# Kernel optimization log

Hardware: AMD Instinct MI355X
Metric: run time of the kernel (lower is better)

The kernel has to match this reference:

```python
import jax, jax.numpy as jnp
import numpy as np

N = 50000      # nodes
E = 250000     # edges
NG = 2500      # graphs
H = 32         # atom_dim
ND = 32        # node feature dim
ED = 16        # edge feature dim
CONV_N = 3     # message passing steps
EMB_STEPS = 3  # Set2Set processing steps


def setup_inputs() -> dict:
    key = jax.random.key(0)
    ks = jax.random.split(key, 16)
    w = lambda k, shape, s=0.05: jax.random.normal(k, shape, jnp.float32) * s
    return {
        "x": jax.random.normal(ks[0], (N, ND), jnp.float32),
        "edge_index": jax.random.randint(ks[1], (2, E), 0, N),
        "edge_attr": jax.random.normal(ks[2], (E, ED), jnp.float32),
        "batch": jnp.sort(jax.random.randint(ks[3], (N,), 0, NG)),
        "lin_w": w(ks[4], (ND, H)), "lin_b": jnp.zeros((H,), jnp.float32),
        "e_w1": w(ks[5], (ED, 2 * H)), "e_b1": jnp.zeros((2 * H,), jnp.float32),
        "e_w2": w(ks[6], (2 * H, H * H)), "e_b2": jnp.zeros((H * H,), jnp.float32),
        "gru_w_ih": w(ks[7], (3 * H, H)), "gru_w_hh": w(ks[8], (3 * H, H)),
        "gru_b_ih": jnp.zeros((3 * H,), jnp.float32), "gru_b_hh": jnp.zeros((3 * H,), jnp.float32),
        "lstm_w_ih": w(ks[9], (4 * H, 2 * H)), "lstm_w_hh": w(ks[10], (4 * H, H)),
        "lstm_b_ih": jnp.zeros((4 * H,), jnp.float32), "lstm_b_hh": jnp.zeros((4 * H,), jnp.float32),
        "pred_w": w(ks[11], (2 * H, 1)), "pred_b": jnp.zeros((1,), jnp.float32),
    }


def _mpnn_forward(x, edge_attr, lin_w, lin_b, e_w1, e_b1, e_w2, e_b2,
                  gru_w_ih, gru_w_hh, gru_b_ih, gru_b_hh,
                  lstm_w_ih, lstm_w_hh, lstm_b_ih, lstm_b_hh,
                  pred_w, pred_b, edge_index, batch):
    src, dst = edge_index[0], edge_index[1]
    # initial node embedding: relu(Linear(node_dim -> atom_dim))
    out = jax.nn.relu(x @ lin_w + lin_b)            # [N, H]
    h = out                                         # GRU hidden state [N, H]

    # edge-conditioned weights (edge MLP output is constant across conv steps)
    e_h = jax.nn.relu(edge_attr @ e_w1 + e_b1)      # [E, 2H]
    W_e = (e_h @ e_w2 + e_b2).reshape(E, H, H)      # [E, H, H]

    # mean-aggregation denominator per target node
    deg = jax.ops.segment_sum(jnp.ones((E,), out.dtype), dst, num_segments=N)
    denom = jnp.maximum(deg, 1.0)[:, None]          # [N, 1]

    for _ in range(CONV_N):
        # NNConv message: m_e = x_src @ W_e, mean-scattered to dst
        msg = jnp.einsum('eh,eho->eo', out[src], W_e)                   # [E, H]
        agg = jax.ops.segment_sum(msg, dst, num_segments=N) / denom     # [N, H]
        m = jax.nn.relu(agg)
        # single GRU cell step (seq_len=1)
        gi = m @ gru_w_ih.T + gru_b_ih              # [N, 3H]
        gh = h @ gru_w_hh.T + gru_b_hh              # [N, 3H]
        i_r, i_z, i_n = jnp.split(gi, 3, axis=-1)
        h_r, h_z, h_n = jnp.split(gh, 3, axis=-1)
        r = jax.nn.sigmoid(i_r + h_r)
        z = jax.nn.sigmoid(i_z + h_z)
        n = jnp.tanh(i_n + r * h_n)
        h = (1.0 - z) * n + z * h
        out = h

    # Set2Set pooling over graphs (only last embedding used, residual='last')
    q_star = jnp.zeros((NG, 2 * H), out.dtype)
    hl = jnp.zeros((NG, H), out.dtype)
    cl = jnp.zeros((NG, H), out.dtype)
    for _ in range(EMB_STEPS):
        g = q_star @ lstm_w_ih.T + lstm_b_ih + hl @ lstm_w_hh.T + lstm_b_hh  # [NG, 4H]
        gi_, gf_, gg_, go_ = jnp.split(g, 4, axis=-1)
        i_g = jax.nn.sigmoid(gi_)
        f_g = jax.nn.sigmoid(gf_)
        g_g = jnp.tanh(gg_)
        o_g = jax.nn.sigmoid(go_)
        cl = f_g * cl + i_g * g_g
        hl = o_g * jnp.tanh(cl)
        q = hl                                       # [NG, H]
        e = jnp.sum(out * q[batch], axis=-1)         # [N]
        e_max = jax.ops.segment_max(e, batch, num_segments=NG)
        e_exp = jnp.exp(e - e_max[batch])
        e_den = jax.ops.segment_sum(e_exp, batch, num_segments=NG)
        a = e_exp / e_den[batch]                     # softmax within each graph
        r_pool = jax.ops.segment_sum(a[:, None] * out, batch, num_segments=NG)  # [NG, H]
        q_star = jnp.concatenate([q, r_pool], axis=-1)

    pred = q_star @ pred_w + pred_b                  # [NG, 1]
    return pred.reshape(-1)


def reference(x, edge_index, edge_attr, batch, lin_w, lin_b, e_w1, e_b1, e_w2, e_b2,
              gru_w_ih, gru_w_hh, gru_b_ih, gru_b_hh,
              lstm_w_ih, lstm_w_hh, lstm_b_ih, lstm_b_hh, pred_w, pred_b):
    return _mpnn_forward(x, edge_attr, lin_w, lin_b, e_w1, e_b1, e_w2, e_b2,
                         gru_w_ih, gru_w_hh, gru_b_ih, gru_b_hh,
                         lstm_w_ih, lstm_w_hh, lstm_b_ih, lstm_b_hh,
                         pred_w, pred_b, edge_index, batch)
```

## Files before the change

### kernel.cpp

```cpp
#include <hip/hip_runtime.h>
#include <hip/hip_bf16.h>

namespace {
constexpr int kN = 50000;
constexpr int kE = 250000;
constexpr int kG = 2500;
constexpr int NB = 8;

__device__ __forceinline__ float sigmoidf_(float x) { return 1.0f / (1.0f + expf(-x)); }

__global__ void k_starts(const int* __restrict__ batch, int* __restrict__ starts) {
  int g = blockIdx.x * blockDim.x + threadIdx.x;
  if (g > kG) return;
  int lo = 0, hi = kN;
  while (lo < hi) {
    int mid = (lo + hi) >> 1;
    if (batch[mid] < g) lo = mid + 1; else hi = mid;
  }
  starts[g] = lo;
}

__global__ __launch_bounds__(256) void k_node_init(const float* __restrict__ x,
                                                   const float* __restrict__ lin_w,
                                                   const float* __restrict__ lin_b,
                                                   float* __restrict__ h) {
  __shared__ float ws[32 * 32];
  __shared__ float bs[32];
  for (int i = threadIdx.x; i < 1024; i += 256) ws[i] = lin_w[i];
  if (threadIdx.x < 32) bs[threadIdx.x] = lin_b[threadIdx.x];
  __syncthreads();
  int n = blockIdx.x * 256 + threadIdx.x;
  if (n >= kN) return;
  float xv[32];
  const float4* xp = (const float4*)(x + (size_t)n * 32);
#pragma unroll
  for (int i = 0; i < 8; ++i) {
    float4 v = xp[i];
    xv[4 * i + 0] = v.x; xv[4 * i + 1] = v.y; xv[4 * i + 2] = v.z; xv[4 * i + 3] = v.w;
  }
  float acc[32];
#pragma unroll
  for (int o = 0; o < 32; ++o) acc[o] = bs[o];
  for (int i = 0; i < 32; ++i) {
    float a = xv[i];
    const float4* wr = (const float4*)&ws[i * 32];
#pragma unroll
    for (int o4 = 0; o4 < 8; ++o4) {
      float4 w = wr[o4];
      acc[4 * o4 + 0] = fmaf(a, w.x, acc[4 * o4 + 0]);
      acc[4 * o4 + 1] = fmaf(a, w.y, acc[4 * o4 + 1]);
      acc[4 * o4 + 2] = fmaf(a, w.z, acc[4 * o4 + 2]);
      acc[4 * o4 + 3] = fmaf(a, w.w, acc[4 * o4 + 3]);
    }
  }
  float4* hp = (float4*)(h + (size_t)n * 32);
#pragma unroll
  for (int i = 0; i < 8; ++i) {
    float4 v;
    v.x = fmaxf(acc[4 * i + 0], 0.f);
    v.y = fmaxf(acc[4 * i + 1], 0.f);
    v.z = fmaxf(acc[4 * i + 2], 0.f);
    v.w = fmaxf(acc[4 * i + 3], 0.f);
    hp[i] = v;
  }
}

__global__ __launch_bounds__(256) void k_edge_h(const float* __restrict__ ea,
                                                const float* __restrict__ w1,
                                                const float* __restrict__ b1,
                                                const int* __restrict__ pos_of_e,
                                                float* __restrict__ ehs) {
  __shared__ float ws[16 * 64];
  __shared__ float bs[64];
  for (int i = threadIdx.x; i < 1024; i += 256) ws[i] = w1[i];
  if (threadIdx.x < 64) bs[threadIdx.x] = b1[threadIdx.x];
  __syncthreads();
  int e = blockIdx.x * 256 + threadIdx.x;
  if (e >= kE) return;
  float av[16];
  const float4* ap = (const float4*)(ea + (size_t)e * 16);
#pragma unroll
  for (int i = 0; i < 4; ++i) {
    float4 v = ap[i];
    av[4 * i + 0] = v.x; av[4 * i + 1] = v.y; av[4 * i + 2] = v.z; av[4 * i + 3] = v.w;
  }
  float acc[64];
#pragma unroll
  for (int o = 0; o < 64; ++o) acc[o] = bs[o];
  for (int i = 0; i < 16; ++i) {
    float a = av[i];
    const float4* wr = (const float4*)&ws[i * 64];
#pragma unroll
    for (int o4 = 0; o4 < 16; ++o4) {
      float4 w = wr[o4];
      acc[4 * o4 + 0] = fmaf(a, w.x, acc[4 * o4 + 0]);
      acc[4 * o4 + 1] = fmaf(a, w.y, acc[4 * o4 + 1]);
      acc[4 * o4 + 2] = fmaf(a, w.z, acc[4 * o4 + 2]);
      acc[4 * o4 + 3] = fmaf(a, w.w, acc[4 * o4 + 3]);
    }
  }
  float4* op = (float4*)(ehs + (size_t)pos_of_e[e] * 64);
#pragma unroll
  for (int i = 0; i < 16; ++i) {
    float4 v;
    v.x = fmaxf(acc[4 * i + 0], 0.f);
    v.y = fmaxf(acc[4 * i + 1], 0.f);
    v.z = fmaxf(acc[4 * i + 2], 0.f);
    v.w = fmaxf(acc[4 * i + 3], 0.f);
    op[i] = v;
  }
}

__global__ void k_hist2(const int* __restrict__ src, const int* __restrict__ dst,
                        int* __restrict__ cnt_s, int* __restrict__ cnt_d) {
  int e = blockIdx.x * blockDim.x + threadIdx.x;
  if (e < kE) {
    atomicAdd(&cnt_s[src[e]], 1);
    atomicAdd(&cnt_d[dst[e]], 1);
  }
}

__global__ __launch_bounds__(1024) void k_scan2(const int* __restrict__ cnt_s, int* __restrict__ offs_s,
                                                const int* __restrict__ cnt_d, int* __restrict__ offs_d) {
  const int* cnt = blockIdx.x ? cnt_d : cnt_s;
  int* offs = blockIdx.x ? offs_d : offs_s;
  __shared__ int wsum[16];
  __shared__ int wpre[16];
  __shared__ int carry_s;
  const int tid = threadIdx.x;
  const int lane = tid & 63, wv = tid >> 6;
  if (tid == 0) carry_s = 0;
  __syncthreads();
  for (int base = 0; base < kN; base += 1024) {
    int i = base + tid;
    int v = (i < kN) ? cnt[i] : 0;
    int x = v;
#pragma unroll
    for (int d = 1; d < 64; d <<= 1) {
      int t = __shfl_up(x, d, 64);
      if (lane >= d) x += t;
    }
    if (lane == 63) wsum[wv] = x;
    __syncthreads();
    if (wv == 0) {
      int y = (lane < 16) ? wsum[lane] : 0;
#pragma unroll
      for (int d = 1; d < 16; d <<= 1) {
        int t = __shfl_up(y, d, 64);
        if (lane >= d && lane < 16) y += t;
      }
      if (lane < 16) wpre[lane] = y - wsum[lane];
    }
    __syncthreads();
    int carry = carry_s;
    if (i < kN) offs[i] = carry + wpre[wv] + (x - v);
    __syncthreads();
    if (tid == 0) carry_s = carry + wpre[15] + wsum[15];
    __syncthreads();
  }
  if (tid == 0) offs[kN] = carry_s;
}

__global__ void k_scatter_s(const int* __restrict__ src, const int* __restrict__ dst,
                            const int* __restrict__ offs, int* __restrict__ cur,
                            unsigned char* __restrict__ es_nl, int* __restrict__ es_dst,
                            int* __restrict__ pos_of_e) {
  int e = blockIdx.x * blockDim.x + threadIdx.x;
  if (e >= kE) return;
  int s = src[e];
  int pos = offs[s] + atomicAdd(&cur[s], 1);
  es_nl[pos] = (unsigned char)(s & (NB - 1));
  es_dst[pos] = dst[e];
  pos_of_e[e] = pos;
}

__global__ void k_scatter_d(const int* __restrict__ es_dst, const int* __restrict__ offs_d,
                            int* __restrict__ cur_d, int* __restrict__ ed_pos) {
  int ei = blockIdx.x * blockDim.x + threadIdx.x;
  if (ei >= kE) return;
  int d = es_dst[ei];
  int pd = offs_d[d] + atomicAdd(&cur_d[d], 1);
  ed_pos[pd] = ei;
}

__global__ void k_w2t(const float* __restrict__ w2, float* __restrict__ w2t) {
  int i = blockIdx.x * 256 + threadIdx.x;
  if (i >= 65536) return;
  int k = i & 63, oa = i >> 6;
  int o = oa & 31, a = oa >> 5;
  w2t[i] = w2[(size_t)k * 1024 + a * 32 + o];
}

__global__ __launch_bounds__(256, 4) void k_conv3(const float* __restrict__ h,
                                                  const float* __restrict__ ehs,
                                                  const float* __restrict__ w2t,
                                                  const float* __restrict__ b2,
                                                  const unsigned char* __restrict__ es_nl,
                                                  const int* __restrict__ offs,
                                                  float* __restrict__ msgbuf) {
  __shared__ float Ts[NB][32][36];
  __shared__ float hs[NB][32];
  __shared__ float hb2[NB][32];
  const int n0 = blockIdx.x * NB;
  const int t = threadIdx.x;
  const int nloc = t >> 5, o32 = t & 31;
  hs[nloc][o32] = h[(size_t)(n0 + nloc) * 32 + o32];
  __syncthreads();
  {
    float a0 = 0.f;
#pragma unroll 8
    for (int a = 0; a < 32; ++a) a0 = fmaf(hs[nloc][a], b2[a * 32 + o32], a0);
    hb2[nloc][o32] = a0;
  }
  const int og = t >> 3;
  const int kq = t & 7;
  const int es = offs[n0], ee = offs[n0 + NB];
  const float* wp = w2t + og * 64 + kq * 4;

  for (int kh = 0; kh < 2; ++kh) {
    float4 acc[NB];
#pragma unroll
    for (int n = 0; n < NB; ++n) acc[n] = make_float4(0.f, 0.f, 0.f, 0.f);
    const float* wph = wp + kh * 32;
#pragma unroll 2
    for (int a4 = 0; a4 < 8; ++a4) {
      const float* wa = wph + (size_t)(a4 * 4) * 2048;
      float4 w0 = *(const float4*)(wa);
      float4 w1 = *(const float4*)(wa + 2048);
      float4 w2v = *(const float4*)(wa + 4096);
      float4 w3 = *(const float4*)(wa + 6144);
#pragma unroll
      for (int n = 0; n < NB; ++n) {
        float4 hv = *(const float4*)&hs[n][a4 * 4];
        acc[n].x = fmaf(hv.x, w0.x, acc[n].x); acc[n].y = fmaf(hv.x, w0.y, acc[n].y);
        acc[n].z = fmaf(hv.x, w0.z, acc[n].z); acc[n].w = fmaf(hv.x, w0.w, acc[n].w);
        acc[n].x = fmaf(hv.y, w1.x, acc[n].x); acc[n].y = fmaf(hv.y, w1.y, acc[n].y);
        acc[n].z = fmaf(hv.y, w1.z, acc[n].z); acc[n].w = fmaf(hv.y, w1.w, acc[n].w);
        acc[n].x = fmaf(hv.z, w2v.x, acc[n].x); acc[n].y = fmaf(hv.z, w2v.y, acc[n].y);
        acc[n].z = fmaf(hv.z, w2v.z, acc[n].z); acc[n].w = fmaf(hv.z, w2v.w, acc[n].w);
        acc[n].x = fmaf(hv.w, w3.x, acc[n].x); acc[n].y = fmaf(hv.w, w3.y, acc[n].y);
        acc[n].z = fmaf(hv.w, w3.z, acc[n].z); acc[n].w = fmaf(hv.w, w3.w, acc[n].w);
      }
    }
    if (kh) __syncthreads();
#pragma unroll
    for (int n = 0; n < NB; ++n) *(float4*)&Ts[n][og][kq * 4] = acc[n];
    __syncthreads();
    const int kg = t >> 5;
#pragma unroll 2
    for (int ei = es + kg; ei < ee; ei += 8) {
      const int nl = es_nl[ei];
      const float ehv = ehs[(size_t)ei * 64 + kh * 32 + o32];
      float m = kh ? msgbuf[(size_t)ei * 32 + o32] : hb2[nl][o32];
      const float* tp = &Ts[nl][o32][0];
#pragma unroll
      for (int j4 = 0; j4 < 8; ++j4) {
        float4 tv = *(const float4*)(tp + j4 * 4);
        m = fmaf(__shfl(ehv, j4 * 4 + 0, 32), tv.x, m);
        m = fmaf(__shfl(ehv, j4 * 4 + 1, 32), tv.y, m);
        m = fmaf(__shfl(ehv, j4 * 4 + 2, 32), tv.z, m);
        m = fmaf(__shfl(ehv, j4 * 4 + 3, 32), tv.w, m);
      }
      msgbuf[(size_t)ei * 32 + o32] = m;
    }
  }
}

__global__ __launch_bounds__(256) void k_agg(const float* __restrict__ msgbuf,
                                             const int* __restrict__ ed_pos,
                                             const int* __restrict__ offs_d,
                                             float* __restrict__ m_out) {
  int d = blockIdx.x * 8 + (threadIdx.x >> 5);
  if (d >= kN) return;
  int o = threadIdx.x & 31;
  int s = offs_d[d], e = offs_d[d + 1];
  float acc = 0.f;
  int j = s;
  for (; j + 1 < e; j += 2) {
    int p0 = ed_pos[j], p1 = ed_pos[j + 1];
    acc += msgbuf[(size_t)p0 * 32 + o] + msgbuf[(size_t)p1 * 32 + o];
  }
  if (j < e) acc += msgbuf[(size_t)ed_pos[j] * 32 + o];
  float dn = (float)(e - s);
  if (dn < 1.f) dn = 1.f;
  m_out[(size_t)d * 32 + o] = fmaxf(acc / dn, 0.f);
}

__global__ __launch_bounds__(256) void k_gru(float* __restrict__ h, const float* __restrict__ m_in,
                                             const float* __restrict__ Wih, const float* __restrict__ Whh,
                                             const float* __restrict__ bih, const float* __restrict__ bhh) {
  __shared__ float wih_s[96 * 32];
  __shared__ float whh_s[96 * 32];
  __shared__ float bih_s[96], bhh_s[96];
  for (int i = threadIdx.x; i < 96 * 32; i += 256) { wih_s[i] = Wih[i]; whh_s[i] = Whh[i]; }
  for (int i = threadIdx.x; i < 96; i += 256) { bih_s[i] = bih[i]; bhh_s[i] = bhh[i]; }
  __syncthreads();
  int n = blockIdx.x * 256 + threadIdx.x;
  if (n >= kN) return;
  float m[32], hv[32];
  const float4* ap = (const float4*)(m_in + (size_t)n * 32);
  const float4* hp = (const float4*)(h + (size_t)n * 32);
#pragma unroll
  for (int i = 0; i < 8; ++i) {
    float4 a = ap[i];
    m[4 * i + 0] = a.x; m[4 * i + 1] = a.y; m[4 * i + 2] = a.z; m[4 * i + 3] = a.w;
    float4 b = hp[i];
    hv[4 * i + 0] = b.x; hv[4 * i + 1] = b.y; hv[4 * i + 2] = b.z; hv[4 * i + 3] = b.w;
  }
  float rr[32], zz[32];
#pragma unroll 4
  for (int j = 0; j < 32; ++j) {
    float accA = bih_s[j], accB = bhh_s[j];
    const float4* wi = (const float4*)&wih_s[j * 32];
    const float4* wh = (const float4*)&whh_s[j * 32];
#pragma unroll
    for (int i = 0; i < 8; ++i) {
      float4 a = wi[i], b = wh[i];
      accA = fmaf(m[4 * i + 0], a.x, accA); accA = fmaf(m[4 * i + 1], a.y, accA);
      accA = fmaf(m[4 * i + 2], a.z, accA); accA = fmaf(m[4 * i + 3], a.w, accA);
      accB = fmaf(hv[4 * i + 0], b.x, accB); accB = fmaf(hv[4 * i + 1], b.y, accB);
      accB = fmaf(hv[4 * i + 2], b.z, accB); accB = fmaf(hv[4 * i + 3], b.w, accB);
    }
    rr[j] = sigmoidf_(accA + accB);
  }
#pragma unroll 4
  for (int j = 0; j < 32; ++j) {
    int row = 32 + j;
    float accA = bih_s[row], accB = bhh_s[row];
    const float4* wi = (const float4*)&wih_s[row * 32];
    const float4* wh = (const float4*)&whh_s[row * 32];
#pragma unroll
    for (int i = 0; i < 8; ++i) {
      float4 a = wi[i], b = wh[i];
      accA = fmaf(m[4 * i + 0], a.x, accA); accA = fmaf(m[4 * i + 1], a.y, accA);
      accA = fmaf(m[4 * i + 2], a.z, accA); accA = fmaf(m[4 * i + 3], a.w, accA);
      accB = fmaf(hv[4 * i + 0], b.x, accB); accB = fmaf(hv[4 * i + 1], b.y, accB);
      accB = fmaf(hv[4 * i + 2], b.z, accB); accB = fmaf(hv[4 * i + 3], b.w, accB);
    }
    zz[j] = sigmoidf_(accA + accB);
  }
#pragma unroll 4
  for (int j = 0; j < 32; ++j) {
    int row = 64 + j;
    float accA = bih_s[row], accB = bhh_s[row];
    const float4* wi = (const float4*)&wih_s[row * 32];
    const float4* wh = (const float4*)&whh_s[row * 32];
#pragma unroll
    for (int i = 0; i < 8; ++i) {
      float4 a = wi[i], b = wh[i];
      accA = fmaf(m[4 * i + 0], a.x, accA); accA = fmaf(m[4 * i + 1], a.y, accA);
      accA = fmaf(m[4 * i + 2], a.z, accA); accA = fmaf(m[4 * i + 3], a.w, accA);
      accB = fmaf(hv[4 * i + 0], b.x, accB); accB = fmaf(hv[4 * i + 1], b.y, accB);
      accB = fmaf(hv[4 * i + 2], b.z, accB); accB = fmaf(hv[4 * i + 3], b.w, accB);
    }
    float ng = tanhf(accA + rr[j] * accB);
    zz[j] = (1.f - zz[j]) * ng + zz[j] * hv[j];
  }
  float4* hw = (float4*)(h + (size_t)n * 32);
#pragma unroll
  for (int i = 0; i < 8; ++i)
    hw[i] = make_float4(zz[4 * i + 0], zz[4 * i + 1], zz[4 * i + 2], zz[4 * i + 3]);
}

__global__ __launch_bounds__(256) void k_s2s(const float* __restrict__ h,
                                             const int* __restrict__ starts,
                                             const float* __restrict__ lwih,
                                             const float* __restrict__ lwhh,
                                             const float* __restrict__ lbih,
                                             const float* __restrict__ lbhh,
                                             const float* __restrict__ pw,
                                             const float* __restrict__ pb,
                                             float* __restrict__ out) {
  __shared__ float wih_s[128][65];
  __shared__ float whh_s[128][33];
  __shared__ float bsum[128];
  for (int i = threadIdx.x; i < 128 * 64; i += 256) wih_s[i >> 6][i & 63] = lwih[i];
  for (int i = threadIdx.x; i < 128 * 32; i += 256) whh_s[i >> 5][i & 31] = lwhh[i];
  for (int i = threadIdx.x; i < 128; i += 256) bsum[i] = lbih[i] + lbhh[i];
  __syncthreads();
  const int g = blockIdx.x * 4 + (threadIdx.x >> 6);
  if (g >= kG) return;
  const int lane = threadIdx.x & 63;
  const int o = lane & 31;
  const int r1 = lane, r2 = lane + 64;
  const int s = starts[g], e = starts[g + 1];
  float c = 0.f, hl = 0.f, rp = 0.f;
  for (int step = 0; step < 3; ++step) {
    float v1 = bsum[r1], v2 = bsum[r2];
    for (int i = 0; i < 32; ++i) {
      float hli = __shfl(hl, i, 64);
      float rpi = __shfl(rp, i, 64);
      v1 = fmaf(wih_s[r1][i], hli, v1);
      v1 = fmaf(wih_s[r1][32 + i], rpi, v1);
      v1 = fmaf(whh_s[r1][i], hli, v1);
      v2 = fmaf(wih_s[r2][i], hli, v2);
      v2 = fmaf(wih_s[r2][32 + i], rpi, v2);
      v2 = fmaf(whh_s[r2][i], hli, v2);
    }
    float fg = sigmoidf_(__shfl(v1, 32 + o, 64));
    float og_ = sigmoidf_(__shfl(v2, 32 + o, 64));
    float ig = sigmoidf_(v1);
    float gg = tanhf(v2);
    c = fg * c + ig * gg;
    hl = og_ * tanhf(c);
    float q = __shfl(hl, o, 64);
    float mx = -3.0e38f;
    for (int nn = s; nn < e; nn += 2) {
      int n = nn + (lane >> 5);
      float val = (n < e) ? h[(size_t)n * 32 + o] * q : 0.f;
#pragma unroll
      for (int d = 16; d; d >>= 1) val += __shfl_xor(val, d, 32);
      if (n < e) mx = fmaxf(mx, val);
    }
    mx = fmaxf(mx, __shfl_xor(mx, 32, 64));
    float den = 0.f, racc = 0.f;
    for (int nn = s; nn < e; nn += 2) {
      int n = nn + (lane >> 5);
      float hvo = 0.f, val = 0.f;
      if (n < e) { hvo = h[(size_t)n * 32 + o]; val = hvo * q; }
#pragma unroll
      for (int d = 16; d; d >>= 1) val += __shfl_xor(val, d, 32);
      if (n < e) { float p = expf(val - mx); den += p; racc = fmaf(p, hvo, racc); }
    }
    den += __shfl_xor(den, 32, 64);
    racc += __shfl_xor(racc, 32, 64);
    rp = (e > s) ? racc / den : 0.f;
  }
  float acc = __shfl(hl, o, 64) * pw[o] + rp * pw[32 + o];
#pragma unroll
  for (int d = 16; d; d >>= 1) acc += __shfl_xor(acc, d, 32);
  if (lane == 0) out[g] = acc + pb[0];
}

}

extern "C" void kernel_launch(void* const* d_in, const int* in_sizes, int n_in,
                              void* d_out, int out_size, void* d_ws, size_t ws_size,
                              hipStream_t stream) {
  const float* x     = (const float*)d_in[0];
  const int*   eidx  = (const int*)d_in[1];
  const float* eattr = (const float*)d_in[2];
  const int*   batch = (const int*)d_in[3];
  const float* lin_w = (const float*)d_in[4];
  const float* lin_b = (const float*)d_in[5];
  const float* e_w1  = (const float*)d_in[6];
  const float* e_b1  = (const float*)d_in[7];
  const float* e_w2  = (const float*)d_in[8];
  const float* e_b2  = (const float*)d_in[9];
  const float* gwih  = (const float*)d_in[10];
  const float* gwhh  = (const float*)d_in[11];
  const float* gbih  = (const float*)d_in[12];
  const float* gbhh  = (const float*)d_in[13];
  const float* lwih  = (const float*)d_in[14];
  const float* lwhh  = (const float*)d_in[15];
  const float* lbih  = (const float*)d_in[16];
  const float* lbhh  = (const float*)d_in[17];
  const float* pw    = (const float*)d_in[18];
  const float* pb    = (const float*)d_in[19];
  const int* srcp = eidx;
  const int* dstp = eidx + kE;

  float* ws = (float*)d_ws;
  size_t off = 0;
  auto alloc = [&](size_t nel) {
    float* p = ws + off;
    off += (nel + 255) & ~(size_t)255;
    return p;
  };
  float* hbuf   = alloc((size_t)kN * 32);
  float* mbuf   = alloc((size_t)kN * 32);
  float* ehs    = alloc((size_t)kE * 64);
  float* msgbuf = alloc((size_t)kE * 32);
  float* w2t    = alloc(65536);
  int* starts   = (int*)alloc(kG + 1);
  int* cnt_s    = (int*)alloc(kN);
  int* cnt_d    = (int*)alloc(kN);
  int* cur_s    = (int*)alloc(kN);
  int* cur_d    = (int*)alloc(kN);
  int* offs_s   = (int*)alloc(kN + 1);
  int* offs_d   = (int*)alloc(kN + 1);
  int* es_dst   = (int*)alloc(kE);
  int* pos_of_e = (int*)alloc(kE);
  int* ed_pos   = (int*)alloc(kE);
  unsigned char* es_nl = (unsigned char*)alloc((kE + 3) / 4);
  if (ws_size / 4 < off) return;

  hipMemsetAsync(cnt_s, 0, (size_t)kN * 4, stream);
  hipMemsetAsync(cnt_d, 0, (size_t)kN * 4, stream);
  hipMemsetAsync(cur_s, 0, (size_t)kN * 4, stream);
  hipMemsetAsync(cur_d, 0, (size_t)kN * 4, stream);

  k_starts<<<(kG + 1 + 255) / 256, 256, 0, stream>>>(batch, starts);
  k_node_init<<<(kN + 255) / 256, 256, 0, stream>>>(x, lin_w, lin_b, hbuf);
  k_hist2<<<(kE + 255) / 256, 256, 0, stream>>>(srcp, dstp, cnt_s, cnt_d);
  k_scan2<<<2, 1024, 0, stream>>>(cnt_s, offs_s, cnt_d, offs_d);
  k_scatter_s<<<(kE + 255) / 256, 256, 0, stream>>>(srcp, dstp, offs_s, cur_s, es_nl, es_dst,
                                                    pos_of_e);
  k_edge_h<<<(kE + 255) / 256, 256, 0, stream>>>(eattr, e_w1, e_b1, pos_of_e, ehs);
  k_scatter_d<<<(kE + 255) / 256, 256, 0, stream>>>(es_dst, offs_d, cur_d, ed_pos);
  k_w2t<<<65536 / 256, 256, 0, stream>>>(e_w2, w2t);

  for (int step = 0; step < 3; ++step) {
    k_conv3<<<kN / NB, 256, 0, stream>>>(hbuf, ehs, w2t, e_b2, es_nl, offs_s, msgbuf);
    k_agg<<<(kN + 7) / 8, 256, 0, stream>>>(msgbuf, ed_pos, offs_d, mbuf);
    k_gru<<<(kN + 255) / 256, 256, 0, stream>>>(hbuf, mbuf, gwih, gwhh, gbih, gbhh);
  }

  k_s2s<<<(kG + 3) / 4, 256, 0, stream>>>(hbuf, starts, lwih, lwhh, lbih, lbhh, pw, pb,
                                          (float*)d_out);
}
```

Baseline: 1.004 ms.

## Restructure conv kernel with per-node edge loops, register-held transforms, coalesced edge_h writes

The conv kernel now assigns each warp one source node. Each lane keeps its row of the per-node transformed weight tile in registers and loops over that node's edges, reading edge hidden vectors as float4 instead of broadcasting them through shuffles. The shared tile uses an XOR swizzle, and weight loads are software-prefetched one step ahead. Edge-hidden computation now iterates in sorted edge order so its writes are coalesced, the aggregation loads destination indices cooperatively and shuffles them, and the GRU reads weights straight from global or cache instead of staging them in shared memory. The risk is load imbalance across warps when nodes have uneven degrees, and more register pressure.

```diff
diff --git a/kernel.cpp b/kernel.cpp
--- a/kernel.cpp
+++ b/kernel.cpp
@@ -68,15 +68,16 @@
 __global__ __launch_bounds__(256) void k_edge_h(const float* __restrict__ ea,
                                                 const float* __restrict__ w1,
                                                 const float* __restrict__ b1,
-                                                const int* __restrict__ pos_of_e,
+                                                const int* __restrict__ es_e,
                                                 float* __restrict__ ehs) {
   __shared__ float ws[16 * 64];
   __shared__ float bs[64];
   for (int i = threadIdx.x; i < 1024; i += 256) ws[i] = w1[i];
   if (threadIdx.x < 64) bs[threadIdx.x] = b1[threadIdx.x];
   __syncthreads();
-  int e = blockIdx.x * 256 + threadIdx.x;
-  if (e >= kE) return;
+  int pos = blockIdx.x * 256 + threadIdx.x;
+  if (pos >= kE) return;
+  int e = es_e[pos];
   float av[16];
   const float4* ap = (const float4*)(ea + (size_t)e * 16);
 #pragma unroll
@@ -99,7 +100,7 @@
       acc[4 * o4 + 3] = fmaf(a, w.w, acc[4 * o4 + 3]);
     }
   }
-  float4* op = (float4*)(ehs + (size_t)pos_of_e[e] * 64);
+  float4* op = (float4*)(ehs + (size_t)pos * 64);
 #pragma unroll
   for (int i = 0; i < 16; ++i) {
     float4 v;
@@ -163,15 +164,13 @@
 
 __global__ void k_scatter_s(const int* __restrict__ src, const int* __restrict__ dst,
                             const int* __restrict__ offs, int* __restrict__ cur,
-                            unsigned char* __restrict__ es_nl, int* __restrict__ es_dst,
-                            int* __restrict__ pos_of_e) {
+                            int* __restrict__ es_e, int* __restrict__ es_dst) {
   int e = blockIdx.x * blockDim.x + threadIdx.x;
   if (e >= kE) return;
   int s = src[e];
   int pos = offs[s] + atomicAdd(&cur[s], 1);
-  es_nl[pos] = (unsigned char)(s & (NB - 1));
+  es_e[pos] = e;
   es_dst[pos] = dst[e];
-  pos_of_e[e] = pos;
 }
 
 __global__ void k_scatter_d(const int* __restrict__ es_dst, const int* __restrict__ offs_d,
@@ -191,77 +190,87 @@
   w2t[i] = w2[(size_t)k * 1024 + a * 32 + o];
 }
 
-__global__ __launch_bounds__(256, 4) void k_conv3(const float* __restrict__ h,
+__global__ __launch_bounds__(256, 4) void k_conv4(const float* __restrict__ h,
                                                   const float* __restrict__ ehs,
                                                   const float* __restrict__ w2t,
                                                   const float* __restrict__ b2,
-                                                  const unsigned char* __restrict__ es_nl,
                                                   const int* __restrict__ offs,
                                                   float* __restrict__ msgbuf) {
   __shared__ float Ts[NB][32][36];
-  __shared__ float hs[NB][32];
-  __shared__ float hb2[NB][32];
   const int n0 = blockIdx.x * NB;
   const int t = threadIdx.x;
-  const int nloc = t >> 5, o32 = t & 31;
-  hs[nloc][o32] = h[(size_t)(n0 + nloc) * 32 + o32];
-  __syncthreads();
+  const int tb_o = t & 31;
+  const int tb_k = t >> 5;
+  const int eg_n = t >> 5;
+  const int eg_o = t & 31;
+  const int gs = offs[n0 + eg_n], ge = offs[n0 + eg_n + 1];
+
+  float hb2r = 0.f;
   {
-    float a0 = 0.f;
+    const float* hp = h + (size_t)(n0 + eg_n) * 32;
 #pragma unroll 8
-    for (int a = 0; a < 32; ++a) a0 = fmaf(hs[nloc][a], b2[a * 32 + o32], a0);
-    hb2[nloc][o32] = a0;
-  }
-  const int og = t >> 3;
-  const int kq = t & 7;
-  const int es = offs[n0], ee = offs[n0 + NB];
-  const float* wp = w2t + og * 64 + kq * 4;
+    for (int a = 0; a < 32; ++a) hb2r = fmaf(hp[a], b2[a * 32 + eg_o], hb2r);
+  }
+
+  const float* wp = w2t + tb_o * 64 + tb_k * 4;
+  const int tswz = tb_o >> 3;
+  const int rswz = eg_o >> 3;
 
   for (int kh = 0; kh < 2; ++kh) {
     float4 acc[NB];
 #pragma unroll
     for (int n = 0; n < NB; ++n) acc[n] = make_float4(0.f, 0.f, 0.f, 0.f);
     const float* wph = wp + kh * 32;
-#pragma unroll 2
+    float4 wa0 = *(const float4*)(wph);
+    float4 wa1 = *(const float4*)(wph + 2048);
+    float4 wa2 = *(const float4*)(wph + 4096);
+    float4 wa3 = *(const float4*)(wph + 6144);
+#pragma unroll
     for (int a4 = 0; a4 < 8; ++a4) {
-      const float* wa = wph + (size_t)(a4 * 4) * 2048;
-      float4 w0 = *(const float4*)(wa);
-      float4 w1 = *(const float4*)(wa + 2048);
-      float4 w2v = *(const float4*)(wa + 4096);
-      float4 w3 = *(const float4*)(wa + 6144);
+      const float* nx = wph + (size_t)((a4 < 7 ? a4 + 1 : a4) * 4) * 2048;
+      float4 wb0 = *(const float4*)(nx);
+      float4 wb1 = *(const float4*)(nx + 2048);
+      float4 wb2 = *(const float4*)(nx + 4096);
+      float4 wb3 = *(const float4*)(nx + 6144);
 #pragma unroll
       for (int n = 0; n < NB; ++n) {
-        float4 hv = *(const float4*)&hs[n][a4 * 4];
-        acc[n].x = fmaf(hv.x, w0.x, acc[n].x); acc[n].y = fmaf(hv.x, w0.y, acc[n].y);
-        acc[n].z = fmaf(hv.x, w0.z, acc[n].z); acc[n].w = fmaf(hv.x, w0.w, acc[n].w);
-        acc[n].x = fmaf(hv.y, w1.x, acc[n].x); acc[n].y = fmaf(hv.y, w1.y, acc[n].y);
-        acc[n].z = fmaf(hv.y, w1.z, acc[n].z); acc[n].w = fmaf(hv.y, w1.w, acc[n].w);
-        acc[n].x = fmaf(hv.z, w2v.x, acc[n].x); acc[n].y = fmaf(hv.z, w2v.y, acc[n].y);
-        acc[n].z = fmaf(hv.z, w2v.z, acc[n].z); acc[n].w = fmaf(hv.z, w2v.w, acc[n].w);
-        acc[n].x = fmaf(hv.w, w3.x, acc[n].x); acc[n].y = fmaf(hv.w, w3.y, acc[n].y);
-        acc[n].z = fmaf(hv.w, w3.z, acc[n].z); acc[n].w = fmaf(hv.w, w3.w, acc[n].w);
+        float4 hv = *(const float4*)(h + (size_t)(n0 + n) * 32 + a4 * 4);
+        acc[n].x = fmaf(hv.x, wa0.x, acc[n].x); acc[n].y = fmaf(hv.x, wa0.y, acc[n].y);
+        acc[n].z = fmaf(hv.x, wa0.z, acc[n].z); acc[n].w = fmaf(hv.x, wa0.w, acc[n].w);
+        acc[n].x = fmaf(hv.y, wa1.x, acc[n].x); acc[n].y = fmaf(hv.y, wa1.y, acc[n].y);
+        acc[n].z = fmaf(hv.y, wa1.z, acc[n].z); acc[n].w = fmaf(hv.y, wa1.w, acc[n].w);
+        acc[n].x = fmaf(hv.z, wa2.x, acc[n].x); acc[n].y = fmaf(hv.z, wa2.y, acc[n].y);
+        acc[n].z = fmaf(hv.z, wa2.z, acc[n].z); acc[n].w = fmaf(hv.z, wa2.w, acc[n].w);
+        acc[n].x = fmaf(hv.w, wa3.x, acc[n].x); acc[n].y = fmaf(hv.w, wa3.y, acc[n].y);
+        acc[n].z = fmaf(hv.w, wa3.z, acc[n].z); acc[n].w = fmaf(hv.w, wa3.w, acc[n].w);
       }
+      wa0 = wb0; wa1 = wb1; wa2 = wb2; wa3 = wb3;
     }
     if (kh) __syncthreads();
 #pragma unroll
-    for (int n = 0; n < NB; ++n) *(float4*)&Ts[n][og][kq * 4] = acc[n];
+    for (int n = 0; n < NB; ++n)
+      *(float4*)&Ts[n][tb_o][(tb_k ^ tswz) * 4] = acc[n];
     __syncthreads();
-    const int kg = t >> 5;
-#pragma unroll 2
-    for (int ei = es + kg; ei < ee; ei += 8) {
-      const int nl = es_nl[ei];
-      const float ehv = ehs[(size_t)ei * 64 + kh * 32 + o32];
-      float m = kh ? msgbuf[(size_t)ei * 32 + o32] : hb2[nl][o32];
-      const float* tp = &Ts[nl][o32][0];
-#pragma unroll
-      for (int j4 = 0; j4 < 8; ++j4) {
-        float4 tv = *(const float4*)(tp + j4 * 4);
-        m = fmaf(__shfl(ehv, j4 * 4 + 0, 32), tv.x, m);
-        m = fmaf(__shfl(ehv, j4 * 4 + 1, 32), tv.y, m);
-        m = fmaf(__shfl(ehv, j4 * 4 + 2, 32), tv.z, m);
-        m = fmaf(__shfl(ehv, j4 * 4 + 3, 32), tv.w, m);
+
+    if (gs < ge) {
+      float4 kv[8];
+#pragma unroll
+      for (int kq = 0; kq < 8; ++kq)
+        kv[kq] = *(const float4*)&Ts[eg_n][eg_o][(kq ^ rswz) * 4];
+      for (int ei = gs; ei < ge; ++ei) {
+        const float* ehp = ehs + (size_t)ei * 64 + kh * 32;
+        float m0 = kh ? msgbuf[(size_t)ei * 32 + eg_o] : hb2r;
+        float m1 = 0.f, m2 = 0.f, m3 = 0.f;
+#pragma unroll
+        for (int kq = 0; kq < 8; ++kq) {
+          float4 eq = *(const float4*)(ehp + kq * 4);
+          m0 = fmaf(eq.x, kv[kq].x, m0);
+          m1 = fmaf(eq.y, kv[kq].y, m1);
+          m2 = fmaf(eq.z, kv[kq].z, m2);
+          m3 = fmaf(eq.w, kv[kq].w, m3);
+        }
+        msgbuf[(size_t)ei * 32 + eg_o] = (m0 + m1) + (m2 + m3);
       }
-      msgbuf[(size_t)ei * 32 + o32] = m;
     }
   }
 }
@@ -275,12 +284,14 @@
   int o = threadIdx.x & 31;
   int s = offs_d[d], e = offs_d[d + 1];
   float acc = 0.f;
-  int j = s;
-  for (; j + 1 < e; j += 2) {
-    int p0 = ed_pos[j], p1 = ed_pos[j + 1];
-    acc += msgbuf[(size_t)p0 * 32 + o] + msgbuf[(size_t)p1 * 32 + o];
-  }
-  if (j < e) acc += msgbuf[(size_t)ed_pos[j] * 32 + o];
+  for (int base = s; base < e; base += 32) {
+    int cnt = e - base; if (cnt > 32) cnt = 32;
+    int p = (base + o < e) ? ed_pos[base + o] : 0;
+    for (int j = 0; j < cnt; ++j) {
+      int pj = __shfl(p, j, 32);
+      acc += msgbuf[(size_t)pj * 32 + o];
+    }
+  }
   float dn = (float)(e - s);
   if (dn < 1.f) dn = 1.f;
   m_out[(size_t)d * 32 + o] = fmaxf(acc / dn, 0.f);
@@ -289,12 +300,6 @@
 __global__ __launch_bounds__(256) void k_gru(float* __restrict__ h, const float* __restrict__ m_in,
                                              const float* __restrict__ Wih, const float* __restrict__ Whh,
                                              const float* __restrict__ bih, const float* __restrict__ bhh) {
-  __shared__ float wih_s[96 * 32];
-  __shared__ float whh_s[96 * 32];
-  __shared__ float bih_s[96], bhh_s[96];
-  for (int i = threadIdx.x; i < 96 * 32; i += 256) { wih_s[i] = Wih[i]; whh_s[i] = Whh[i]; }
-  for (int i = threadIdx.x; i < 96; i += 256) { bih_s[i] = bih[i]; bhh_s[i] = bhh[i]; }
-  __syncthreads();
   int n = blockIdx.x * 256 + threadIdx.x;
   if (n >= kN) return;
   float m[32], hv[32];
@@ -310,9 +315,9 @@
   float rr[32], zz[32];
 #pragma unroll 4
   for (int j = 0; j < 32; ++j) {
-    float accA = bih_s[j], accB = bhh_s[j];
-    const float4* wi = (const float4*)&wih_s[j * 32];
-    const float4* wh = (const float4*)&whh_s[j * 32];
+    float accA = bih[j], accB = bhh[j];
+    const float4* wi = (const float4*)(Wih + (size_t)j * 32);
+    const float4* wh = (const float4*)(Whh + (size_t)j * 32);
 #pragma unroll
     for (int i = 0; i < 8; ++i) {
       float4 a = wi[i], b = wh[i];
@@ -326,9 +331,9 @@
 #pragma unroll 4
   for (int j = 0; j < 32; ++j) {
     int row = 32 + j;
-    float accA = bih_s[row], accB = bhh_s[row];
-    const float4* wi = (const float4*)&wih_s[row * 32];
-    const float4* wh = (const float4*)&whh_s[row * 32];
+    float accA = bih[row], accB = bhh[row];
+    const float4* wi = (const float4*)(Wih + (size_t)row * 32);
+    const float4* wh = (const float4*)(Whh + (size_t)row * 32);
 #pragma unroll
     for (int i = 0; i < 8; ++i) {
       float4 a = wi[i], b = wh[i];
@@ -342,9 +347,9 @@
 #pragma unroll 4
   for (int j = 0; j < 32; ++j) {
     int row = 64 + j;
-    float accA = bih_s[row], accB = bhh_s[row];
-    const float4* wi = (const float4*)&wih_s[row * 32];
-    const float4* wh = (const float4*)&whh_s[row * 32];
+    float accA = bih[row], accB = bhh[row];
+    const float4* wi = (const float4*)(Wih + (size_t)row * 32);
+    const float4* wh = (const float4*)(Whh + (size_t)row * 32);
 #pragma unroll
     for (int i = 0; i < 8; ++i) {
       float4 a = wi[i], b = wh[i];
@@ -479,10 +484,9 @@
   int* cur_d    = (int*)alloc(kN);
   int* offs_s   = (int*)alloc(kN + 1);
   int* offs_d   = (int*)alloc(kN + 1);
+  int* es_e     = (int*)alloc(kE);
   int* es_dst   = (int*)alloc(kE);
-  int* pos_of_e = (int*)alloc(kE);
   int* ed_pos   = (int*)alloc(kE);
-  unsigned char* es_nl = (unsigned char*)alloc((kE + 3) / 4);
   if (ws_size / 4 < off) return;
 
   hipMemsetAsync(cnt_s, 0, (size_t)kN * 4, stream);
@@ -494,14 +498,13 @@
   k_node_init<<<(kN + 255) / 256, 256, 0, stream>>>(x, lin_w, lin_b, hbuf);
   k_hist2<<<(kE + 255) / 256, 256, 0, stream>>>(srcp, dstp, cnt_s, cnt_d);
   k_scan2<<<2, 1024, 0, stream>>>(cnt_s, offs_s, cnt_d, offs_d);
-  k_scatter_s<<<(kE + 255) / 256, 256, 0, stream>>>(srcp, dstp, offs_s, cur_s, es_nl, es_dst,
-                                                    pos_of_e);
-  k_edge_h<<<(kE + 255) / 256, 256, 0, stream>>>(eattr, e_w1, e_b1, pos_of_e, ehs);
+  k_scatter_s<<<(kE + 255) / 256, 256, 0, stream>>>(srcp, dstp, offs_s, cur_s, es_e, es_dst);
+  k_edge_h<<<(kE + 255) / 256, 256, 0, stream>>>(eattr, e_w1, e_b1, es_e, ehs);
   k_scatter_d<<<(kE + 255) / 256, 256, 0, stream>>>(es_dst, offs_d, cur_d, ed_pos);
   k_w2t<<<65536 / 256, 256, 0, stream>>>(e_w2, w2t);
 
   for (int step = 0; step < 3; ++step) {
-    k_conv3<<<kN / NB, 256, 0, stream>>>(hbuf, ehs, w2t, e_b2, es_nl, offs_s, msgbuf);
+    k_conv4<<<kN / NB, 256, 0, stream>>>(hbuf, ehs, w2t, e_b2, offs_s, msgbuf);
     k_agg<<<(kN + 7) / 8, 256, 0, stream>>>(msgbuf, ed_pos, offs_d, mbuf);
     k_gru<<<(kN + 255) / 256, 256, 0, stream>>>(hbuf, mbuf, gwih, gwhh, gbih, gbhh);
   }
```

New measurement: 1.868 ms. 86.1% more time.

## Replace shuffle-broadcast edge loop with vector loads, batch index loads in aggregation

Applied to the files above, without the earlier changes.

The conv kernel's per-edge inner loop used to broadcast each edge-hidden value with 32 shuffles. It now has every lane load the edge-hidden row directly as float4 vectors and accumulate into four independent partial sums, which removes the shuffle cost and shortens the FMA dependency chain. The edge MLP kernel now iterates in sorted (CSR) order through an es_e index, so its output writes are contiguous while its input reads become a gather. The aggregation kernel loads up to 32 edge positions per wavefront at once and broadcasts them with shuffles instead of issuing serial index loads. The trade-off is redundant per-lane global loads of the same ehs row and a changed floating-point summation order.

```diff
diff --git a/kernel.cpp b/kernel.cpp
--- a/kernel.cpp
+++ b/kernel.cpp
@@ -68,15 +68,16 @@
 __global__ __launch_bounds__(256) void k_edge_h(const float* __restrict__ ea,
                                                 const float* __restrict__ w1,
                                                 const float* __restrict__ b1,
-                                                const int* __restrict__ pos_of_e,
+                                                const int* __restrict__ es_e,
                                                 float* __restrict__ ehs) {
   __shared__ float ws[16 * 64];
   __shared__ float bs[64];
   for (int i = threadIdx.x; i < 1024; i += 256) ws[i] = w1[i];
   if (threadIdx.x < 64) bs[threadIdx.x] = b1[threadIdx.x];
   __syncthreads();
-  int e = blockIdx.x * 256 + threadIdx.x;
-  if (e >= kE) return;
+  int pos = blockIdx.x * 256 + threadIdx.x;
+  if (pos >= kE) return;
+  int e = es_e[pos];
   float av[16];
   const float4* ap = (const float4*)(ea + (size_t)e * 16);
 #pragma unroll
@@ -99,7 +100,7 @@
       acc[4 * o4 + 3] = fmaf(a, w.w, acc[4 * o4 + 3]);
     }
   }
-  float4* op = (float4*)(ehs + (size_t)pos_of_e[e] * 64);
+  float4* op = (float4*)(ehs + (size_t)pos * 64);
 #pragma unroll
   for (int i = 0; i < 16; ++i) {
     float4 v;
@@ -163,15 +164,15 @@
 
 __global__ void k_scatter_s(const int* __restrict__ src, const int* __restrict__ dst,
                             const int* __restrict__ offs, int* __restrict__ cur,
-                            unsigned char* __restrict__ es_nl, int* __restrict__ es_dst,
-                            int* __restrict__ pos_of_e) {
+                            int* __restrict__ es_e, int* __restrict__ es_dst,
+                            unsigned char* __restrict__ es_nl) {
   int e = blockIdx.x * blockDim.x + threadIdx.x;
   if (e >= kE) return;
   int s = src[e];
   int pos = offs[s] + atomicAdd(&cur[s], 1);
+  es_e[pos] = e;
+  es_dst[pos] = dst[e];
   es_nl[pos] = (unsigned char)(s & (NB - 1));
-  es_dst[pos] = dst[e];
-  pos_of_e[e] = pos;
 }
 
 __global__ void k_scatter_d(const int* __restrict__ es_dst, const int* __restrict__ offs_d,
@@ -191,7 +192,7 @@
   w2t[i] = w2[(size_t)k * 1024 + a * 32 + o];
 }
 
-__global__ __launch_bounds__(256, 4) void k_conv3(const float* __restrict__ h,
+__global__ __launch_bounds__(256, 4) void k_conv5(const float* __restrict__ h,
                                                   const float* __restrict__ ehs,
                                                   const float* __restrict__ w2t,
                                                   const float* __restrict__ b2,
@@ -216,6 +217,7 @@
   const int kq = t & 7;
   const int es = offs[n0], ee = offs[n0 + NB];
   const float* wp = w2t + og * 64 + kq * 4;
+  const int kg = t >> 5;
 
   for (int kh = 0; kh < 2; ++kh) {
     float4 acc[NB];
@@ -246,22 +248,23 @@
 #pragma unroll
     for (int n = 0; n < NB; ++n) *(float4*)&Ts[n][og][kq * 4] = acc[n];
     __syncthreads();
-    const int kg = t >> 5;
-#pragma unroll 2
+
     for (int ei = es + kg; ei < ee; ei += 8) {
       const int nl = es_nl[ei];
-      const float ehv = ehs[(size_t)ei * 64 + kh * 32 + o32];
-      float m = kh ? msgbuf[(size_t)ei * 32 + o32] : hb2[nl][o32];
+      const float* ehp = ehs + (size_t)ei * 64 + kh * 32;
+      float m0 = kh ? msgbuf[(size_t)ei * 32 + o32] : hb2[nl][o32];
+      float m1 = 0.f, m2 = 0.f, m3 = 0.f;
       const float* tp = &Ts[nl][o32][0];
 #pragma unroll
-      for (int j4 = 0; j4 < 8; ++j4) {
-        float4 tv = *(const float4*)(tp + j4 * 4);
-        m = fmaf(__shfl(ehv, j4 * 4 + 0, 32), tv.x, m);
-        m = fmaf(__shfl(ehv, j4 * 4 + 1, 32), tv.y, m);
-        m = fmaf(__shfl(ehv, j4 * 4 + 2, 32), tv.z, m);
-        m = fmaf(__shfl(ehv, j4 * 4 + 3, 32), tv.w, m);
+      for (int kq2 = 0; kq2 < 8; ++kq2) {
+        float4 eq = *(const float4*)(ehp + kq2 * 4);
+        float4 tv = *(const float4*)(tp + kq2 * 4);
+        m0 = fmaf(eq.x, tv.x, m0);
+        m1 = fmaf(eq.y, tv.y, m1);
+        m2 = fmaf(eq.z, tv.z, m2);
+        m3 = fmaf(eq.w, tv.w, m3);
       }
-      msgbuf[(size_t)ei * 32 + o32] = m;
+      msgbuf[(size_t)ei * 32 + o32] = (m0 + m1) + (m2 + m3);
     }
   }
 }
@@ -275,12 +278,14 @@
   int o = threadIdx.x & 31;
   int s = offs_d[d], e = offs_d[d + 1];
   float acc = 0.f;
-  int j = s;
-  for (; j + 1 < e; j += 2) {
-    int p0 = ed_pos[j], p1 = ed_pos[j + 1];
-    acc += msgbuf[(size_t)p0 * 32 + o] + msgbuf[(size_t)p1 * 32 + o];
-  }
-  if (j < e) acc += msgbuf[(size_t)ed_pos[j] * 32 + o];
+  for (int base = s; base < e; base += 32) {
+    int cnt = e - base; if (cnt > 32) cnt = 32;
+    int p = (base + o < e) ? ed_pos[base + o] : 0;
+    for (int j = 0; j < cnt; ++j) {
+      int pj = __shfl(p, j, 32);
+      acc += msgbuf[(size_t)pj * 32 + o];
+    }
+  }
   float dn = (float)(e - s);
   if (dn < 1.f) dn = 1.f;
   m_out[(size_t)d * 32 + o] = fmaxf(acc / dn, 0.f);
@@ -479,8 +484,8 @@
   int* cur_d    = (int*)alloc(kN);
   int* offs_s   = (int*)alloc(kN + 1);
   int* offs_d   = (int*)alloc(kN + 1);
+  int* es_e     = (int*)alloc(kE);
   int* es_dst   = (int*)alloc(kE);
-  int* pos_of_e = (int*)alloc(kE);
   int* ed_pos   = (int*)alloc(kE);
   unsigned char* es_nl = (unsigned char*)alloc((kE + 3) / 4);
   if (ws_size / 4 < off) return;
@@ -494,14 +499,14 @@
   k_node_init<<<(kN + 255) / 256, 256, 0, stream>>>(x, lin_w, lin_b, hbuf);
   k_hist2<<<(kE + 255) / 256, 256, 0, stream>>>(srcp, dstp, cnt_s, cnt_d);
   k_scan2<<<2, 1024, 0, stream>>>(cnt_s, offs_s, cnt_d, offs_d);
-  k_scatter_s<<<(kE + 255) / 256, 256, 0, stream>>>(srcp, dstp, offs_s, cur_s, es_nl, es_dst,
-                                                    pos_of_e);
-  k_edge_h<<<(kE + 255) / 256, 256, 0, stream>>>(eattr, e_w1, e_b1, pos_of_e, ehs);
+  k_scatter_s<<<(kE + 255) / 256, 256, 0, stream>>>(srcp, dstp, offs_s, cur_s, es_e, es_dst,
+                                                    es_nl);
+  k_edge_h<<<(kE + 255) / 256, 256, 0, stream>>>(eattr, e_w1, e_b1, es_e, ehs);
   k_scatter_d<<<(kE + 255) / 256, 256, 0, stream>>>(es_dst, offs_d, cur_d, ed_pos);
   k_w2t<<<65536 / 256, 256, 0, stream>>>(e_w2, w2t);
 
   for (int step = 0; step < 3; ++step) {
-    k_conv3<<<kN / NB, 256, 0, stream>>>(hbuf, ehs, w2t, e_b2, es_nl, offs_s, msgbuf);
+    k_conv5<<<kN / NB, 256, 0, stream>>>(hbuf, ehs, w2t, e_b2, es_nl, offs_s, msgbuf);
     k_agg<<<(kN + 7) / 8, 256, 0, stream>>>(msgbuf, ed_pos, offs_d, mbuf);
     k_gru<<<(kN + 255) / 256, 256, 0, stream>>>(hbuf, mbuf, gwih, gwhh, gbih, gbhh);
   }
```

After: 979.8 us. 1.02x faster.
